# Kernel optimization log

Hardware: AMD Instinct MI355X
Metric: run time of the kernel (lower is better)

## Reference

```python
import jax, jax.numpy as jnp
from jax import lax
import numpy as np

# CenterNet decode config
B, C, H, W = 16, 80, 128, 128  # batch, classes, feature-map H/W (512 input / down_ratio 4)
K = 100                        # top-K detections per image
DOWN = 4.0                     # down_ratio: feature-map coords -> input-image coords


def setup_inputs() -> dict:
    key = jax.random.key(0)
    k1, k2, k3 = jax.random.split(key, 3)
    return {
        "output_heatmap": jax.random.normal(k1, (B, C, H, W), dtype=jnp.float32),
        "output_bbox": jax.random.uniform(k2, (B, 2, H, W), dtype=jnp.float32) * 32.0,  # wh head
        "output_offset": jax.random.uniform(k3, (B, 2, H, W), dtype=jnp.float32),       # sub-pixel offset head
        "image_id": jnp.arange(B, dtype=jnp.int32),
    }


def reference(output_heatmap, output_bbox, output_offset, image_id):
    # 1) peak scores
    hm = jax.nn.sigmoid(output_heatmap)  # [B,C,H,W]
    # 2) 3x3 maxpool NMS: keep only local maxima
    hmax = lax.reduce_window(hm, -jnp.inf, lax.max,
                             window_dimensions=(1, 1, 3, 3),
                             window_strides=(1, 1, 1, 1),
                             padding='SAME')
    hm = jnp.where(hmax == hm, hm, jnp.zeros((), hm.dtype))
    # 3) per-image top-K over all classes and positions
    scores, inds = lax.top_k(hm.reshape(B, C * H * W), K)  # [B,K]
    cls = (inds // (H * W)).astype(jnp.float32)             # [B,K]
    sp = inds % (H * W)                                     # spatial index in [0, H*W)
    ys = (sp // W).astype(jnp.float32)
    xs = (sp % W).astype(jnp.float32)
    # 4) sparse gather of offset and wh at the K peak locations
    off = jnp.take_along_axis(output_offset.reshape(B, 2, H * W), sp[:, None, :], axis=2)  # [B,2,K]
    wh = jnp.take_along_axis(output_bbox.reshape(B, 2, H * W), sp[:, None, :], axis=2)     # [B,2,K]
    cx = xs + off[:, 0]
    cy = ys + off[:, 1]
    w = wh[:, 0]
    h = wh[:, 1]
    # 5) decode to corner boxes in input-image coordinates
    boxes = jnp.stack([cx - w / 2, cy - h / 2, cx + w / 2, cy + h / 2], axis=-1) * DOWN  # [B,K,4]
    img = jnp.broadcast_to(image_id[:, None].astype(jnp.float32), (B, K))
    # detections: [image_id, x1, y1, x2, y2, score, class] -> [B,K,7]
    det = jnp.concatenate([img[..., None], boxes, scores[..., None], cls[..., None]], axis=-1)
    return det
```

## Files before the change

kernel.cpp:

```cpp
#include <hip/hip_runtime.h>

#define BB 16
#define CC 80
#define HWs 16384
#define KK 100
#define NBIN 2048
#define BCAP 2304
#define SBCAP 128

#define OFF_BHIST 0
#define OFF_CUT   131072
#define OFF_PBCNT 131136
#define OFF_PSCNT 136256
#define OFF_REC   141376
#define OFF_SURV  11937856

__device__ __forceinline__ unsigned okey(float f) {
    unsigned u = __float_as_uint(f);
    return (u & 0x80000000u) ? ~u : (u | 0x80000000u);
}

__global__ __launch_bounds__(256) void zero_hist_kernel(int4* __restrict__ bhist) {
    int i = blockIdx.x * 256 + threadIdx.x;
    if (i < BB * NBIN / 4) bhist[i] = make_int4(0, 0, 0, 0);
}

__global__ __launch_bounds__(256) void nms_kernel(const float* __restrict__ hm,
                                                  unsigned* __restrict__ rec,
                                                  int* __restrict__ pbcnt,
                                                  int* __restrict__ bhist) {
    __shared__ int hist[NBIN];
    __shared__ int wbase[4];
    const int plane = blockIdx.x;
    const int b = plane / CC;
    const int c = plane - b * CC;
    const int t = threadIdx.x;
    const int lane = t & 63;
    const int wid = t >> 6;
    const int sx = t & 31;
    const int x0 = sx << 2;
    const int band0 = (t >> 5) << 4;
    const float4* __restrict__ src4 =
        reinterpret_cast<const float4*>(hm + (size_t)plane * HWs);

    for (int i = t; i < NBIN; i += 256) hist[i] = 0;
    __syncthreads();

    auto hmax3 = [&](const float4& a) -> float4 {
        float vm1 = __shfl_up(a.w, 1, 32);
        float vp4 = __shfl_down(a.x, 1, 32);
        if (sx == 0) vm1 = a.x;
        if (sx == 31) vp4 = a.w;
        float4 h;
        h.x = fmaxf(fmaxf(vm1, a.x), a.y);
        h.y = fmaxf(fmaxf(a.x, a.y), a.z);
        h.z = fmaxf(fmaxf(a.y, a.z), a.w);
        h.w = fmaxf(fmaxf(a.z, a.w), vp4);
        return h;
    };

    unsigned* __restrict__ rb = rec + (size_t)plane * BCAP;
    int rbase = 0;

#pragma unroll
    for (int chunk = 0; chunk < 4; ++chunk) {
        const int y0 = band0 + (chunk << 2);

        float4 v[6];
#pragma unroll
        for (int r = 0; r < 6; ++r) {
            int rr = y0 - 1 + r;
            rr = rr < 0 ? 0 : (rr > 127 ? 127 : rr);
            v[r] = src4[(rr << 5) + sx];
        }

        unsigned pmask = 0;
        float4 hm1 = hmax3(v[0]);
        float4 h0  = hmax3(v[1]);
#pragma unroll
        for (int r = 0; r < 4; ++r) {
            float4 hp1 = hmax3(v[r + 2]);
            if (v[r + 1].x >= fmaxf(fmaxf(hm1.x, h0.x), hp1.x)) pmask |= 1u << (r * 4 + 0);
            if (v[r + 1].y >= fmaxf(fmaxf(hm1.y, h0.y), hp1.y)) pmask |= 1u << (r * 4 + 1);
            if (v[r + 1].z >= fmaxf(fmaxf(hm1.z, h0.z), hp1.z)) pmask |= 1u << (r * 4 + 2);
            if (v[r + 1].w >= fmaxf(fmaxf(hm1.w, h0.w), hp1.w)) pmask |= 1u << (r * 4 + 3);
            hm1 = h0; h0 = hp1;
        }

        int cntp = __popc(pmask);
        int sc = cntp;
#pragma unroll
        for (int off = 1; off < 64; off <<= 1) {
            int n = __shfl_up(sc, off, 64);
            if (lane >= off) sc += n;
        }
        if (lane == 63) wbase[wid] = sc;
        __syncthreads();
        int wexcl = 0;
#pragma unroll
        for (int i = 0; i < 4; ++i) if (i < wid) wexcl += wbase[i];
        const int blocktot = wbase[0] + wbase[1] + wbase[2] + wbase[3];
        int w = rbase + wexcl + sc - cntp;

#pragma unroll
        for (int r = 0; r < 4; ++r) {
            float vv0 = v[r + 1].x, vv1 = v[r + 1].y, vv2 = v[r + 1].z, vv3 = v[r + 1].w;
#pragma unroll
            for (int j = 0; j < 4; ++j) {
                if (pmask & (1u << (r * 4 + j))) {
                    float lv = (j == 0) ? vv0 : (j == 1) ? vv1 : (j == 2) ? vv2 : vv3;
                    unsigned bin = okey(lv) >> 21;
                    atomicAdd(&hist[bin], 1);
                    unsigned idx = ((unsigned)c << 14) | ((unsigned)(y0 + r) << 7)
                                 | (unsigned)(x0 + j);
                    if (w < BCAP) rb[w] = (bin << 21) | idx;
                    ++w;
                }
            }
        }
        __syncthreads();
        rbase += blocktot;
    }

    if (t == 0) pbcnt[plane] = rbase > BCAP ? BCAP : rbase;

    for (int i = t; i < NBIN; i += 256) {
        int hv = hist[i];
        if (hv) atomicAdd(&bhist[b * NBIN + i], hv);
    }
}

__global__ __launch_bounds__(256) void cut_kernel(const int* __restrict__ bhist,
                                                  int* __restrict__ cut) {
    __shared__ int csum[256];
    __shared__ int s_cut;
    const int b = blockIdx.x;
    const int t = threadIdx.x;

    int h[8]; int chunk = 0;
#pragma unroll
    for (int j = 0; j < 8; ++j) {
        h[j] = bhist[b * NBIN + (t << 3) + j];
        chunk += h[j];
    }
    csum[t] = chunk;
    if (t == 0) s_cut = 0;
    __syncthreads();
    for (int off = 1; off < 256; off <<= 1) {
        int v = (t + off < 256) ? csum[t + off] : 0;
        __syncthreads();
        csum[t] += v;
        __syncthreads();
    }
    if (csum[0] > KK) {
        int running = (t < 255) ? csum[t + 1] : 0;
        if (csum[t] >= KK && running < KK) {
            for (int j = 7; j >= 0; --j) {
                running += h[j];
                if (running >= KK) { s_cut = (t << 3) + j; break; }
            }
        }
    }
    __syncthreads();
    if (t == 0) cut[b] = s_cut;
}

__global__ __launch_bounds__(256) void filter_kernel(const unsigned* __restrict__ rec,
                                                     const int* __restrict__ pbcnt,
                                                     const int* __restrict__ cut,
                                                     unsigned* __restrict__ surv,
                                                     int* __restrict__ pscnt) {
    __shared__ int s_n;
    const int bx = blockIdx.x;
    const int b = bx / CC;
    const int t = threadIdx.x;
    if (t == 0) s_n = 0;
    __syncthreads();

    int n = pbcnt[bx]; if (n > BCAP) n = BCAP;
    const int cutb = cut[b];
    const unsigned* __restrict__ rb = rec + (size_t)bx * BCAP;
    unsigned* __restrict__ sb = surv + (size_t)bx * SBCAP;
    for (int i = t; i < n; i += 256) {
        unsigned rv = rb[i];
        if ((int)(rv >> 21) >= cutb) {
            int sl = atomicAdd(&s_n, 1);
            if (sl < SBCAP) sb[sl] = rv & 0x1FFFFFu;
        }
    }
    __syncthreads();
    if (t == 0) pscnt[bx] = s_n > SBCAP ? SBCAP : s_n;
}

__global__ __launch_bounds__(256) void topk_kernel(const unsigned* __restrict__ surv,
                                                   const int* __restrict__ pscnt,
                                                   const float* __restrict__ hm,
                                                   const float* __restrict__ bbox,
                                                   const float* __restrict__ offs,
                                                   const int* __restrict__ image_id,
                                                   float* __restrict__ out) {
    __shared__ int lcnt[CC];
    __shared__ unsigned uidx[2048];
    __shared__ unsigned long long list[2048];
    __shared__ int s_n;
    const int b = blockIdx.x;
    const int t = threadIdx.x;
    const float* __restrict__ hb = hm + (size_t)b * CC * HWs;

    if (t < CC) lcnt[t] = pscnt[b * CC + t];
    if (t == 0) s_n = 0;
    __syncthreads();

    for (int s = t; s < CC; s += 256) {
        int cs = lcnt[s]; if (cs > SBCAP) cs = SBCAP;
        if (cs) {
            int base = atomicAdd(&s_n, cs);
            const unsigned* __restrict__ sb = surv + ((size_t)b * CC + s) * SBCAP;
            for (int k = 0; k < cs; ++k)
                if (base + k < 2048) uidx[base + k] = sb[k];
        }
    }
    __syncthreads();
    int n = s_n; if (n > 2048) n = 2048;

    for (int i = t; i < n; i += 256) {
        unsigned idx = uidx[i];
        float lv = hb[idx];
        float s = 1.0f / (1.0f + expf(-lv));
        list[i] = ((unsigned long long)__float_as_uint(s) << 32) | (unsigned)(~idx);
    }
    int P = 128;
    while (P < n) P <<= 1;
    for (int i = n + t; i < P; i += 256) list[i] = 0ull;
    __syncthreads();

    for (int ksz = 2; ksz <= P; ksz <<= 1) {
        for (int j = ksz >> 1; j > 0; j >>= 1) {
            for (int i = t; i < P; i += 256) {
                int ixj = i ^ j;
                if (ixj > i) {
                    unsigned long long a = list[i], bb2 = list[ixj];
                    bool desc = ((i & ksz) == 0);
                    if (desc ? (a < bb2) : (a > bb2)) { list[i] = bb2; list[ixj] = a; }
                }
            }
            __syncthreads();
        }
    }

    if (t < KK) {
        float s = 0.0f; unsigned idx = 0;
        if (t < n) {
            unsigned long long cv = list[t];
            s = __uint_as_float((unsigned)(cv >> 32));
            idx = ~(unsigned)(cv & 0xFFFFFFFFu) & 0x1FFFFFu;
        }
        unsigned sp = idx & (HWs - 1);
        float cls = (float)(idx >> 14);
        float ysf = (float)(sp >> 7);
        float xsf = (float)(sp & 127);
        const float* __restrict__ ob  = offs + (size_t)b * 2 * HWs;
        const float* __restrict__ bbx = bbox + (size_t)b * 2 * HWs;
        float cx = xsf + ob[sp];
        float cy = ysf + ob[HWs + sp];
        float w = bbx[sp];
        float h = bbx[HWs + sp];
        float* row = out + ((size_t)b * KK + t) * 7;
        row[0] = (float)image_id[b];
        row[1] = (cx - w * 0.5f) * 4.0f;
        row[2] = (cy - h * 0.5f) * 4.0f;
        row[3] = (cx + w * 0.5f) * 4.0f;
        row[4] = (cy + h * 0.5f) * 4.0f;
        row[5] = s;
        row[6] = cls;
    }
}

extern "C" void kernel_launch(void* const* d_in, const int* in_sizes, int n_in,
                              void* d_out, int out_size, void* d_ws, size_t ws_size,
                              hipStream_t stream) {
    const float* hm      = (const float*)d_in[0];
    const float* bbox    = (const float*)d_in[1];
    const float* offset  = (const float*)d_in[2];
    const int*   img_id  = (const int*)d_in[3];
    float* out = (float*)d_out;

    char* ws = (char*)d_ws;
    int*      bhist = (int*)(ws + OFF_BHIST);
    int*      cut   = (int*)(ws + OFF_CUT);
    int*      pbcnt = (int*)(ws + OFF_PBCNT);
    int*      pscnt = (int*)(ws + OFF_PSCNT);
    unsigned* rec   = (unsigned*)(ws + OFF_REC);
    unsigned* surv  = (unsigned*)(ws + OFF_SURV);

    zero_hist_kernel<<<32, 256, 0, stream>>>((int4*)bhist);
    nms_kernel<<<BB * CC, 256, 0, stream>>>(hm, rec, pbcnt, bhist);
    cut_kernel<<<BB, 256, 0, stream>>>(bhist, cut);
    filter_kernel<<<BB * CC, 256, 0, stream>>>(rec, pbcnt, cut, surv, pscnt);
    topk_kernel<<<BB, 256, 0, stream>>>(surv, pscnt, hm, bbox, offset, img_id, out);
}
```

Before: 62.33 us.

## Compact NMS peaks via shared-memory atomic slots instead of block prefix scans

```diff
diff --git a/kernel.cpp b/kernel.cpp
--- a/kernel.cpp
+++ b/kernel.cpp
@@ -30,13 +30,12 @@
                                                   int* __restrict__ pbcnt,
                                                   int* __restrict__ bhist) {
     __shared__ int hist[NBIN];
-    __shared__ int wbase[4];
+    __shared__ unsigned sbuf[BCAP];
+    __shared__ int s_n;
     const int plane = blockIdx.x;
     const int b = plane / CC;
     const int c = plane - b * CC;
     const int t = threadIdx.x;
-    const int lane = t & 63;
-    const int wid = t >> 6;
     const int sx = t & 31;
     const int x0 = sx << 2;
     const int band0 = (t >> 5) << 4;
@@ -44,6 +43,7 @@
         reinterpret_cast<const float4*>(hm + (size_t)plane * HWs);
 
     for (int i = t; i < NBIN; i += 256) hist[i] = 0;
+    if (t == 0) s_n = 0;
     __syncthreads();
 
     auto hmax3 = [&](const float4& a) -> float4 {
@@ -59,75 +59,54 @@
         return h;
     };
 
-    unsigned* __restrict__ rb = rec + (size_t)plane * BCAP;
-    int rbase = 0;
-
-#pragma unroll
-    for (int chunk = 0; chunk < 4; ++chunk) {
-        const int y0 = band0 + (chunk << 2);
-
-        float4 v[6];
-#pragma unroll
-        for (int r = 0; r < 6; ++r) {
-            int rr = y0 - 1 + r;
+#pragma unroll
+    for (int chunk = 0; chunk < 2; ++chunk) {
+        const int y0 = band0 + (chunk << 3);
+
+        float4 w[10];
+#pragma unroll
+        for (int i = 0; i < 10; ++i) {
+            int rr = y0 - 1 + i;
             rr = rr < 0 ? 0 : (rr > 127 ? 127 : rr);
-            v[r] = src4[(rr << 5) + sx];
-        }
-
-        unsigned pmask = 0;
-        float4 hm1 = hmax3(v[0]);
-        float4 h0  = hmax3(v[1]);
-#pragma unroll
-        for (int r = 0; r < 4; ++r) {
-            float4 hp1 = hmax3(v[r + 2]);
-            if (v[r + 1].x >= fmaxf(fmaxf(hm1.x, h0.x), hp1.x)) pmask |= 1u << (r * 4 + 0);
-            if (v[r + 1].y >= fmaxf(fmaxf(hm1.y, h0.y), hp1.y)) pmask |= 1u << (r * 4 + 1);
-            if (v[r + 1].z >= fmaxf(fmaxf(hm1.z, h0.z), hp1.z)) pmask |= 1u << (r * 4 + 2);
-            if (v[r + 1].w >= fmaxf(fmaxf(hm1.w, h0.w), hp1.w)) pmask |= 1u << (r * 4 + 3);
-            hm1 = h0; h0 = hp1;
-        }
-
-        int cntp = __popc(pmask);
-        int sc = cntp;
-#pragma unroll
-        for (int off = 1; off < 64; off <<= 1) {
-            int n = __shfl_up(sc, off, 64);
-            if (lane >= off) sc += n;
-        }
-        if (lane == 63) wbase[wid] = sc;
-        __syncthreads();
-        int wexcl = 0;
-#pragma unroll
-        for (int i = 0; i < 4; ++i) if (i < wid) wexcl += wbase[i];
-        const int blocktot = wbase[0] + wbase[1] + wbase[2] + wbase[3];
-        int w = rbase + wexcl + sc - cntp;
-
-#pragma unroll
-        for (int r = 0; r < 4; ++r) {
-            float vv0 = v[r + 1].x, vv1 = v[r + 1].y, vv2 = v[r + 1].z, vv3 = v[r + 1].w;
+            w[i] = src4[(rr << 5) + sx];
+        }
+        __builtin_amdgcn_sched_barrier(0);
+
+        float4 hm1 = hmax3(w[0]);
+        float4 h0  = hmax3(w[1]);
+#pragma unroll
+        for (int r = 0; r < 8; ++r) {
+            float4 hp1 = hmax3(w[r + 2]);
+            float vv[4] = { w[r + 1].x, w[r + 1].y, w[r + 1].z, w[r + 1].w };
+            float mm[4] = { fmaxf(fmaxf(hm1.x, h0.x), hp1.x),
+                            fmaxf(fmaxf(hm1.y, h0.y), hp1.y),
+                            fmaxf(fmaxf(hm1.z, h0.z), hp1.z),
+                            fmaxf(fmaxf(hm1.w, h0.w), hp1.w) };
 #pragma unroll
             for (int j = 0; j < 4; ++j) {
-                if (pmask & (1u << (r * 4 + j))) {
-                    float lv = (j == 0) ? vv0 : (j == 1) ? vv1 : (j == 2) ? vv2 : vv3;
-                    unsigned bin = okey(lv) >> 21;
-                    atomicAdd(&hist[bin], 1);
-                    unsigned idx = ((unsigned)c << 14) | ((unsigned)(y0 + r) << 7)
-                                 | (unsigned)(x0 + j);
-                    if (w < BCAP) rb[w] = (bin << 21) | idx;
-                    ++w;
+                if (vv[j] >= mm[j]) {
+                    int sl = atomicAdd(&s_n, 1);
+                    unsigned bin = okey(vv[j]) >> 21;
+                    unsigned idx = ((unsigned)c << 14)
+                                 | ((unsigned)(y0 + r) << 7) | (unsigned)(x0 + j);
+                    if (sl < BCAP) sbuf[sl] = (bin << 21) | idx;
                 }
             }
-        }
-        __syncthreads();
-        rbase += blocktot;
-    }
-
-    if (t == 0) pbcnt[plane] = rbase > BCAP ? BCAP : rbase;
-
+            hm1 = h0; h0 = hp1;
+        }
+    }
+    __syncthreads();
+    int n = s_n; if (n > BCAP) n = BCAP;
+
+    for (int i = t; i < n; i += 256) atomicAdd(&hist[sbuf[i] >> 21], 1);
+    __syncthreads();
     for (int i = t; i < NBIN; i += 256) {
         int hv = hist[i];
         if (hv) atomicAdd(&bhist[b * NBIN + i], hv);
     }
+    unsigned* __restrict__ rb = rec + (size_t)plane * BCAP;
+    for (int i = t; i < n; i += 256) rb[i] = sbuf[i];
+    if (t == 0) pbcnt[plane] = n;
 }
 
 __global__ __launch_bounds__(256) void cut_kernel(const int* __restrict__ bhist,
```

Result: no change. 62.75 us (+0.7%).
